# Performance work log

Hardware: AMD Instinct MI355X
Metric: run time of the kernel (lower is better)

Reference implementation:

```python
import jax, jax.numpy as jnp
import numpy as np

NUM_HEADS = 8
EPS = 1e-6


def hamilton(a, b):
    # Quaternion (Hamilton) product on the last axis (size 4), broadcasting leading dims.
    aw, ax, ay, az = a[..., 0], a[..., 1], a[..., 2], a[..., 3]
    bw, bx, by, bz = b[..., 0], b[..., 1], b[..., 2], b[..., 3]
    return jnp.stack([
        aw * bw - ax * bx - ay * by - az * bz,
        aw * bx + ax * bw + ay * bz - az * by,
        aw * by - ax * bz + ay * bw + az * bx,
        aw * bz + ax * by - ay * bx + az * bw,
    ], axis=-1)


def setup_inputs() -> dict:
    key = jax.random.key(0)
    ks = jax.random.split(key, 7)
    B, L, E = 2, 384, 512
    s = 1.0 / np.sqrt(E)
    return {
        'x': jax.random.normal(ks[0], (B, L, E), dtype=jnp.float32),
        'Wq': jax.random.normal(ks[1], (E, E), dtype=jnp.float32) * s,
        'Wk': jax.random.normal(ks[2], (E, E), dtype=jnp.float32) * s,
        'Wv': jax.random.normal(ks[3], (E, E), dtype=jnp.float32) * s,
        'Wo': jax.random.normal(ks[4], (E, E), dtype=jnp.float32) * s,
        'dde_w': jax.random.normal(ks[5], (4, 4), dtype=jnp.float32) * 0.5,
        'dde_b': jnp.zeros((4,), dtype=jnp.float32),
    }


def reference(x, Wq, Wk, Wv, Wo, dde_w, dde_b):
    B, L, E = x.shape
    H = NUM_HEADS
    hd = E // H            # head_dim
    c = hd // 4            # quaternion atoms per head

    def proj_quat(W):
        # x @ W^T  -> split heads -> quaternion atoms: (B*H, L, c, 4)
        y = jnp.einsum('ble,fe->blf', x, W)
        y = y.reshape(B, L, H, hd).transpose(0, 2, 1, 3)  # (B,H,L,hd)
        return y.reshape(B * H, L, c, 4)

    q = proj_quat(Wq)
    k = proj_quat(Wk)
    v = proj_quat(Wv)

    # Broadcasted Hamilton product: (BH, L, L, c, 4)
    interference = hamilton(q[:, :, None, :, :], k[:, None, :, :, :])
    norm = jnp.linalg.norm(interference, axis=-1, keepdims=True) + EPS
    spinor = interference / norm

    # Discrete decision gate: mean over atoms -> (BH, L, L, 4) -> sigmoid(linear)
    gate_in = spinor.mean(axis=-2)
    gate = jax.nn.sigmoid(jnp.einsum('blmq,pq->blmp', gate_in, dde_w) + dde_b)
    spinor = spinor * gate[:, :, :, None, :]

    # Value aggregation: Hamilton product with v, summed over key positions j
    ctx = hamilton(spinor, v[:, None, :, :, :]).sum(axis=2)  # (BH, L, c, 4)

    ctx = ctx.reshape(B, H, L, hd).transpose(0, 2, 1, 3).reshape(B, L, E)
    return jnp.einsum('ble,fe->blf', ctx, Wo)
```

## Files before the change

### kernel.cpp

```cpp
#include <hip/hip_runtime.h>
#include <math.h>

#define L_SEQ 384
#define E_DIM 512
#define NHEAD 8
#define NBH   16
#define HD    64
#define LOG2E 1.44269504f

typedef __attribute__((ext_vector_type(8))) __bf16 bf16x8;
typedef __attribute__((ext_vector_type(8))) _Float16 f16x8;
typedef __attribute__((ext_vector_type(4))) float f32x4;

union u4h8 { uint4 u; f16x8 h; };

__device__ __forceinline__ float uniform_f(float v) {
  return __uint_as_float(__builtin_amdgcn_readfirstlane(__float_as_uint(v)));
}

__device__ __forceinline__ unsigned f2bf(float f) {
  unsigned u = __float_as_uint(f);
  return (u + 0x7FFFu + ((u >> 16) & 1u)) >> 16;
}

__device__ __forceinline__ unsigned ror16(unsigned x) { return (x >> 16) | (x << 16); }

__device__ __forceinline__ float dpp_xor1(float x) {
  return __int_as_float(__builtin_amdgcn_mov_dpp(__float_as_int(x), 0xB1, 0xF, 0xF, 0));
}
__device__ __forceinline__ float dpp_xor2(float x) {
  return __int_as_float(__builtin_amdgcn_mov_dpp(__float_as_int(x), 0x4E, 0xF, 0xF, 0));
}
template <int PAT>
__device__ __forceinline__ float quad_bcast(float x) {
  return __int_as_float(__builtin_amdgcn_mov_dpp(__float_as_int(x), PAT, 0xF, 0xF, 0));
}
template <int IMM>
__device__ __forceinline__ float swz_xor(float x) {
  return __int_as_float(__builtin_amdgcn_ds_swizzle(__float_as_int(x), IMM));
}

__device__ __forceinline__ size_t pidx(int row, int k, int Kd) {
  return ((((size_t)(row >> 4) * (Kd >> 5) + (k >> 5)) * 4 + ((k >> 3) & 3)) * 16
          + (row & 15)) * 8 + (k & 7);
}

__global__ __launch_bounds__(256) void to_bf16_all(
    const float* __restrict__ x, const float* __restrict__ Wq,
    const float* __restrict__ Wk, const float* __restrict__ Wv,
    const float* __restrict__ Wo, unsigned short* __restrict__ dst1,
    unsigned short* __restrict__ dst2, float* __restrict__ outz)
{
  int e0 = (blockIdx.x * 256 + threadIdx.x) * 4;
  if (e0 >= 1835008) return;
  if (e0 >= 1441792) {
    *(float4*)(outz + (e0 - 1441792)) = make_float4(0.f, 0.f, 0.f, 0.f);
    return;
  }
  const float* src; unsigned short* d; int s;
  if (e0 < 393216)       { src = x;  s = e0;           d = dst1; }
  else if (e0 < 655360)  { src = Wq; s = e0 - 393216;  d = dst1 + 393216; }
  else if (e0 < 917504)  { src = Wk; s = e0 - 655360;  d = dst1 + 655360; }
  else if (e0 < 1179648) { src = Wv; s = e0 - 917504;  d = dst1 + 917504; }
  else                   { src = Wo; s = e0 - 1179648; d = dst2; }
  float4 v = *(const float4*)(src + s);
  unsigned lo = f2bf(v.x) | (f2bf(v.y) << 16);
  unsigned hi = f2bf(v.z) | (f2bf(v.w) << 16);
  int row = s >> 9, k = s & 511;
  *(uint2*)(d + pidx(row, k, 512)) = make_uint2(lo, hi);
}

__global__ __launch_bounds__(256) void gemm_qkv(
    const __bf16* __restrict__ A, const __bf16* __restrict__ B0,
    const __bf16* __restrict__ B1, const __bf16* __restrict__ B2,
    _Float16* __restrict__ qhh, _Float16* __restrict__ khh,
    _Float16* __restrict__ Z0)
{
  const int z = blockIdx.z;
  const int tid = threadIdx.x;
  const int wave = tid >> 6, lane = tid & 63;
  const int m0 = blockIdx.y * 64 + wave * 16;
  const int n0 = blockIdx.x * 16;
  const int mr = lane & 15, quad = lane >> 4;
  const int KT = 16;

  const __bf16* ap = A + (size_t)(m0 >> 4) * KT * 512 + lane * 8;
  const int n = n0 + mr;

  if (z == 0) {
    const __bf16* bp = B0 + (size_t)(n0 >> 4) * KT * 512 + lane * 8;
    f32x4 acc = (f32x4){0.f, 0.f, 0.f, 0.f};
    #pragma unroll 4
    for (int ks = 0; ks < KT; ++ks) {
      bf16x8 a = *(const bf16x8*)(ap + (size_t)ks * 512);
      bf16x8 b = *(const bf16x8*)(bp + (size_t)ks * 512);
      acc = __builtin_amdgcn_mfma_f32_16x16x32_bf16(a, b, acc, 0, 0, 0);
    }
    #pragma unroll
    for (int r = 0; r < 4; ++r) {
      float val = acc[r];
      float s = val * val;
      s += dpp_xor1(s);
      s += dpp_xor2(s);
      float sc = __builtin_amdgcn_rsqf(fmaxf(s, 1e-30f));
      int m = m0 + quad * 4 + r;
      int b = m / L_SEQ, l = m - b * L_SEQ;
      int row = (b * NHEAD + (n >> 6)) * L_SEQ + l;
      qhh[pidx(row, n & 63, 64)] = (_Float16)(val * sc);
    }
  } else {
    const __bf16* bpk = B1 + (size_t)(n0 >> 4) * KT * 512 + lane * 8;
    const __bf16* bpv = B2 + (size_t)(n0 >> 4) * KT * 512 + lane * 8;
    f32x4 accK = (f32x4){0.f, 0.f, 0.f, 0.f};
    f32x4 accV = (f32x4){0.f, 0.f, 0.f, 0.f};
    #pragma unroll 4
    for (int ks = 0; ks < KT; ++ks) {
      bf16x8 a = *(const bf16x8*)(ap + (size_t)ks * 512);
      bf16x8 bk = *(const bf16x8*)(bpk + (size_t)ks * 512);
      bf16x8 bv = *(const bf16x8*)(bpv + (size_t)ks * 512);
      accK = __builtin_amdgcn_mfma_f32_16x16x32_bf16(a, bk, accK, 0, 0, 0);
      accV = __builtin_amdgcn_mfma_f32_16x16x32_bf16(a, bv, accV, 0, 0, 0);
    }
    const int a_atom = (n & 63) >> 2, comp = n & 3;
    #pragma unroll
    for (int r = 0; r < 4; ++r) {
      float vk = accK[r], vv = accV[r];
      float s = vk * vk;
      s += dpp_xor1(s);
      s += dpp_xor2(s);
      float kn = vk * __builtin_amdgcn_rsqf(fmaxf(s, 1e-30f));
      int m = m0 + quad * 4 + r;
      int b = m / L_SEQ, l = m - b * L_SEQ;
      int bh = b * NHEAD + (n >> 6);
      int row = bh * L_SEQ + l;
      khh[pidx(row, n & 63, 64)] = (_Float16)kn;
      float v0 = quad_bcast<0x00>(vv), v1 = quad_bcast<0x55>(vv);
      float v2 = quad_bcast<0xAA>(vv), v3 = quad_bcast<0xFF>(vv);
      _Float16* zp = Z0 + (size_t)bh * (256 * 384);
      int colb = a_atom * 16 + comp * 4;
      zp[pidx(colb + 0, l, 384)] = (_Float16)(kn * v0);
      zp[pidx(colb + 1, l, 384)] = (_Float16)(kn * v1);
      zp[pidx(colb + 2, l, 384)] = (_Float16)(kn * v2);
      zp[pidx(colb + 3, l, 384)] = (_Float16)(kn * v3);
    }
  }
}

__global__ __launch_bounds__(256) void gate_pv(
    const _Float16* __restrict__ qhh, const _Float16* __restrict__ khh,
    const _Float16* __restrict__ Z0, const float* __restrict__ dde_w,
    const float* __restrict__ dde_b, const __bf16* __restrict__ Wob,
    float* __restrict__ out)
{
  __shared__ _Float16 gbuf[2][4096];
  __shared__ float qs[16][65];
  __shared__ __bf16 ctx_lds[16][72];

  const int tid = threadIdx.x, w = tid >> 6, lane = tid & 63;
  const int mr = lane & 15, quad = lane >> 4;
  const int bh = blockIdx.y, ib = blockIdx.x;
  const int i0 = ib * 16;

  {
    int il = tid >> 4, k4 = (tid & 15) * 4;
    union { uint2 u; _Float16 h[4]; } cv;
    cv.u = *(const uint2*)(qhh + pidx(bh * L_SEQ + i0 + il, k4, 64));
    qs[il][k4 + 0] = (float)cv.h[0]; qs[il][k4 + 1] = (float)cv.h[1];
    qs[il][k4 + 2] = (float)cv.h[2]; qs[il][k4 + 3] = (float)cv.h[3];
  }

  float wn[16], bn[4];
  #pragma unroll
  for (int t = 0; t < 16; ++t) wn[t] = uniform_f(dde_w[t]) * (-LOG2E * 0.0625f);
  #pragma unroll
  for (int c = 0; c < 4; ++c) bn[c] = uniform_f(dde_b[c]) * (-LOG2E);

  u4h8 fr[4][2];
  {
    const _Float16* ap = qhh + ((size_t)(bh * 24 + ib)) * 2 * 512 + lane * 8;
    #pragma unroll
    for (int ks = 0; ks < 2; ++ks) {
      uint4 qa = *(const uint4*)(ap + ks * 512);
      unsigned s0 = ror16(qa.x), s1 = ror16(qa.y), s2 = ror16(qa.z), s3 = ror16(qa.w);
      fr[0][ks].u = make_uint4(qa.x ^ 0x80000000u, qa.y ^ 0x80008000u,
                               qa.z ^ 0x80000000u, qa.w ^ 0x80008000u);
      fr[1][ks].u = make_uint4(s0, s1 ^ 0x00008000u, s2, s3 ^ 0x00008000u);
      fr[2][ks].u = make_uint4(qa.y, qa.x ^ 0x80000000u, qa.w, qa.z ^ 0x80000000u);
      fr[3][ks].u = make_uint4(s1 ^ 0x80000000u, s0, s3 ^ 0x80000000u, s2);
    }
  }

  const int bq = mr >> 2, e = mr & 3;
  unsigned msk[4];
  #pragma unroll
  for (int c = 0; c < 4; ++c)
    msk[c] = ((((0x284Eu >> (c * 4 + bq)) ^ (0xC6A0u >> (c * 4 + e))) & 1u) << 31);

  f32x4 acc[4][4];
  #pragma unroll
  for (int c = 0; c < 4; ++c)
    #pragma unroll
    for (int nt = 0; nt < 4; ++nt) acc[c][nt] = (f32x4){0.f, 0.f, 0.f, 0.f};

  const int jl = w * 16 + mr;
  const int gw = (jl >> 3) * 128 + (jl & 7) + quad * 32;

  u4h8 kbp[2][2];
  {
    const _Float16* bp = khh + ((size_t)(bh * 24 + w)) * 2 * 512 + lane * 8;
    kbp[0][0].h = *(const f16x8*)(bp);
    kbp[0][1].h = *(const f16x8*)(bp + 512);
  }

  #pragma unroll
  for (int ch = 0; ch < 6; ++ch) {
    const int cur = ch & 1, nxt = cur ^ 1;
    u4h8 zb[2][4];
    #pragma unroll
    for (int ks2 = 0; ks2 < 2; ++ks2)
      #pragma unroll
      for (int nt = 0; nt < 4; ++nt)
        zb[ks2][nt].h = *(const f16x8*)(Z0 + (size_t)bh * (256 * 384)
                         + (((size_t)(w * 4 + nt) * 12 + ch * 2 + ks2) * 512) + lane * 8);

    f32x4 accS[4];
    #pragma unroll
    for (int c = 0; c < 4; ++c) {
      accS[c] = (f32x4){0.f, 0.f, 0.f, 0.f};
      accS[c] = __builtin_amdgcn_mfma_f32_16x16x32_f16(fr[c][0].h, kbp[cur][0].h, accS[c], 0, 0, 0);
      accS[c] = __builtin_amdgcn_mfma_f32_16x16x32_f16(fr[c][1].h, kbp[cur][1].h, accS[c], 0, 0, 0);
    }

    if (ch < 5) {
      const _Float16* bp = khh + ((size_t)(bh * 24 + (ch + 1) * 4 + w)) * 2 * 512 + lane * 8;
      kbp[nxt][0].h = *(const f16x8*)(bp);
      kbp[nxt][1].h = *(const f16x8*)(bp + 512);
    }

    #pragma unroll
    for (int r = 0; r < 4; ++r) {
      float S0 = accS[0][r], S1 = accS[1][r], S2 = accS[2][r], S3 = accS[3][r];
      #pragma unroll
      for (int c = 0; c < 4; ++c) {
        float n = bn[c] + wn[c*4+0]*S0 + wn[c*4+1]*S1 + wn[c*4+2]*S2 + wn[c*4+3]*S3;
        float g = __builtin_amdgcn_rcpf(1.f + __builtin_amdgcn_exp2f(n));
        gbuf[cur][c * 1024 + gw + r * 8] = (_Float16)g;
      }
    }
    __syncthreads();

    #pragma unroll
    for (int ks2 = 0; ks2 < 2; ++ks2) {
      #pragma unroll
      for (int c = 0; c < 4; ++c) {
        f16x8 aa = *(const f16x8*)&gbuf[cur][c * 1024 + ks2 * 512 + lane * 8];
        #pragma unroll
        for (int nt = 0; nt < 4; ++nt)
          acc[c][nt] = __builtin_amdgcn_mfma_f32_16x16x32_f16(aa, zb[ks2][nt].h, acc[c][nt], 0, 0, 0);
      }
    }
  }

  #pragma unroll
  for (int nt = 0; nt < 4; ++nt) {
    #pragma unroll
    for (int r = 0; r < 4; ++r) {
      int il = quad * 4 + r;
      float pb[4];
      #pragma unroll
      for (int c = 0; c < 4; ++c) {
        float sq = __uint_as_float(
            __float_as_uint(qs[il][w * 16 + nt * 4 + (bq ^ c)]) ^ msk[c]);
        float v = sq * acc[c][nt][r];
        v += swz_xor<0x101F>(v);
        v += swz_xor<0x201F>(v);
        pb[c] = v;
      }
      float q0 = pb[0] + dpp_xor1(pb[1]);
      float q1 = pb[1] + dpp_xor1(pb[0]);
      float q2 = pb[2] + dpp_xor1(pb[3]);
      float q3 = pb[3] + dpp_xor1(pb[2]);
      float r0 = q0 + dpp_xor2(q2);
      float r1 = q1 + dpp_xor2(q3);
      float r2 = q2 + dpp_xor2(q0);
      float r3 = q3 + dpp_xor2(q1);
      if (mr == 0) {
        ctx_lds[il][w * 16 + nt * 4 + 0] = (__bf16)r0;
        ctx_lds[il][w * 16 + nt * 4 + 1] = (__bf16)r1;
        ctx_lds[il][w * 16 + nt * 4 + 2] = (__bf16)r2;
        ctx_lds[il][w * 16 + nt * 4 + 3] = (__bf16)r3;
      }
    }
  }
  __syncthreads();

  const int bb_ = bh >> 3, hh = bh & 7;
  const int m_base = bb_ * L_SEQ + i0;
  bf16x8 af[2];
  #pragma unroll
  for (int ks2 = 0; ks2 < 2; ++ks2)
    af[ks2] = *(const bf16x8*)&ctx_lds[mr][ks2 * 32 + quad * 8];
  #pragma unroll
  for (int nt2 = 0; nt2 < 8; ++nt2) {
    const int ntile = w * 8 + nt2;
    f32x4 accO = (f32x4){0.f, 0.f, 0.f, 0.f};
    #pragma unroll
    for (int ks2 = 0; ks2 < 2; ++ks2) {
      bf16x8 b = *(const bf16x8*)(Wob + ((size_t)ntile * 16 + hh * 2 + ks2) * 512 + lane * 8);
      accO = __builtin_amdgcn_mfma_f32_16x16x32_bf16(af[ks2], b, accO, 0, 0, 0);
    }
    const int n = ntile * 16 + mr;
    #pragma unroll
    for (int r = 0; r < 4; ++r) {
      int m = m_base + quad * 4 + r;
      __hip_atomic_fetch_add(&out[(size_t)m * E_DIM + n], accO[r],
                             __ATOMIC_RELAXED, __HIP_MEMORY_SCOPE_AGENT);
    }
  }
}

extern "C" void kernel_launch(void* const* d_in, const int* in_sizes, int n_in,
                              void* d_out, int out_size, void* d_ws, size_t ws_size,
                              hipStream_t stream)
{
  const float* x     = (const float*)d_in[0];
  const float* Wq    = (const float*)d_in[1];
  const float* Wk    = (const float*)d_in[2];
  const float* Wv    = (const float*)d_in[3];
  const float* Wo    = (const float*)d_in[4];
  const float* dde_w = (const float*)d_in[5];
  const float* dde_b = (const float*)d_in[6];
  float* out = (float*)d_out;

  char* ws = (char*)d_ws;
  unsigned short* Wob  = (unsigned short*)(ws + 0);
  _Float16* qhh = (_Float16*)(ws + 524288);
  _Float16* khh = (_Float16*)(ws + 1310720);
  _Float16* Z0h = (_Float16*)(ws + 2097152);
  unsigned short* xb  = (unsigned short*)(ws + 6029312);
  unsigned short* Wqb = (unsigned short*)(ws + 6815744);
  unsigned short* Wkb = (unsigned short*)(ws + 7340032);
  unsigned short* Wvb = (unsigned short*)(ws + 7864320);

  to_bf16_all<<<1792, 256, 0, stream>>>(x, Wq, Wk, Wv, Wo, xb, Wob, out);

  gemm_qkv<<<dim3(32, 12, 2), 256, 0, stream>>>(
      (const __bf16*)xb, (const __bf16*)Wqb, (const __bf16*)Wkb, (const __bf16*)Wvb,
      qhh, khh, Z0h);

  gate_pv<<<dim3(24, 16), 256, 0, stream>>>(
      qhh, khh, Z0h, dde_w, dde_b, (const __bf16*)Wob, out);
}
```

Baseline: 101.3 us.

## Split gate_pv key range across two blocks and rebuild query fragments per chunk

The gate_pv grid gains a z dimension of 2, and each block handles half of the key-position chunks (3 of 6). This doubles the block count to fill the GPU better and shorten each block's serial loop. The permuted query fragments are now rebuilt from the two raw loads right before each MFMA group instead of being kept in 8 registers. The launch bound asks for 3 blocks per CU to raise occupancy. It relies on the epilogue accumulating partial outputs atomically into the zeroed output, so output-projection work and atomic traffic double.

```diff
diff --git a/kernel.cpp b/kernel.cpp
--- a/kernel.cpp
+++ b/kernel.cpp
@@ -43,6 +43,24 @@
 __device__ __forceinline__ size_t pidx(int row, int k, int Kd) {
   return ((((size_t)(row >> 4) * (Kd >> 5) + (k >> 5)) * 4 + ((k >> 3) & 3)) * 16
           + (row & 15)) * 8 + (k & 7);
+}
+
+template <int C>
+__device__ __forceinline__ u4h8 build_fr(uint4 qa) {
+  u4h8 f;
+  if (C == 0) {
+    f.u = make_uint4(qa.x ^ 0x80000000u, qa.y ^ 0x80008000u,
+                     qa.z ^ 0x80000000u, qa.w ^ 0x80008000u);
+  } else if (C == 1) {
+    f.u = make_uint4(ror16(qa.x), ror16(qa.y) ^ 0x00008000u,
+                     ror16(qa.z), ror16(qa.w) ^ 0x00008000u);
+  } else if (C == 2) {
+    f.u = make_uint4(qa.y, qa.x ^ 0x80000000u, qa.w, qa.z ^ 0x80000000u);
+  } else {
+    f.u = make_uint4(ror16(qa.y) ^ 0x80000000u, ror16(qa.x),
+                     ror16(qa.w) ^ 0x80000000u, ror16(qa.z));
+  }
+  return f;
 }
 
 __global__ __launch_bounds__(256) void to_bf16_all(
@@ -146,7 +164,7 @@
   }
 }
 
-__global__ __launch_bounds__(256) void gate_pv(
+__global__ __launch_bounds__(256, 3) void gate_pv(
     const _Float16* __restrict__ qhh, const _Float16* __restrict__ khh,
     const _Float16* __restrict__ Z0, const float* __restrict__ dde_w,
     const float* __restrict__ dde_b, const __bf16* __restrict__ Wob,
@@ -158,7 +176,7 @@
 
   const int tid = threadIdx.x, w = tid >> 6, lane = tid & 63;
   const int mr = lane & 15, quad = lane >> 4;
-  const int bh = blockIdx.y, ib = blockIdx.x;
+  const int bh = blockIdx.y, ib = blockIdx.x, jh = blockIdx.z;
   const int i0 = ib * 16;
 
   {
@@ -175,19 +193,11 @@
   #pragma unroll
   for (int c = 0; c < 4; ++c) bn[c] = uniform_f(dde_b[c]) * (-LOG2E);
 
-  u4h8 fr[4][2];
+  uint4 qa[2];
   {
     const _Float16* ap = qhh + ((size_t)(bh * 24 + ib)) * 2 * 512 + lane * 8;
-    #pragma unroll
-    for (int ks = 0; ks < 2; ++ks) {
-      uint4 qa = *(const uint4*)(ap + ks * 512);
-      unsigned s0 = ror16(qa.x), s1 = ror16(qa.y), s2 = ror16(qa.z), s3 = ror16(qa.w);
-      fr[0][ks].u = make_uint4(qa.x ^ 0x80000000u, qa.y ^ 0x80008000u,
-                               qa.z ^ 0x80000000u, qa.w ^ 0x80008000u);
-      fr[1][ks].u = make_uint4(s0, s1 ^ 0x00008000u, s2, s3 ^ 0x00008000u);
-      fr[2][ks].u = make_uint4(qa.y, qa.x ^ 0x80000000u, qa.w, qa.z ^ 0x80000000u);
-      fr[3][ks].u = make_uint4(s1 ^ 0x80000000u, s0, s3 ^ 0x80000000u, s2);
-    }
+    qa[0] = *(const uint4*)(ap);
+    qa[1] = *(const uint4*)(ap + 512);
   }
 
   const int bq = mr >> 2, e = mr & 3;
@@ -207,14 +217,15 @@
 
   u4h8 kbp[2][2];
   {
-    const _Float16* bp = khh + ((size_t)(bh * 24 + w)) * 2 * 512 + lane * 8;
+    const _Float16* bp = khh + ((size_t)(bh * 24 + jh * 12 + w)) * 2 * 512 + lane * 8;
     kbp[0][0].h = *(const f16x8*)(bp);
     kbp[0][1].h = *(const f16x8*)(bp + 512);
   }
 
   #pragma unroll
-  for (int ch = 0; ch < 6; ++ch) {
-    const int cur = ch & 1, nxt = cur ^ 1;
+  for (int ci = 0; ci < 3; ++ci) {
+    const int ch = jh * 3 + ci;
+    const int cur = ci & 1, nxt = cur ^ 1;
     u4h8 zb[2][4];
     #pragma unroll
     for (int ks2 = 0; ks2 < 2; ++ks2)
@@ -224,15 +235,28 @@
                          + (((size_t)(w * 4 + nt) * 12 + ch * 2 + ks2) * 512) + lane * 8);
 
     f32x4 accS[4];
-    #pragma unroll
-    for (int c = 0; c < 4; ++c) {
-      accS[c] = (f32x4){0.f, 0.f, 0.f, 0.f};
-      accS[c] = __builtin_amdgcn_mfma_f32_16x16x32_f16(fr[c][0].h, kbp[cur][0].h, accS[c], 0, 0, 0);
-      accS[c] = __builtin_amdgcn_mfma_f32_16x16x32_f16(fr[c][1].h, kbp[cur][1].h, accS[c], 0, 0, 0);
-    }
-
-    if (ch < 5) {
-      const _Float16* bp = khh + ((size_t)(bh * 24 + (ch + 1) * 4 + w)) * 2 * 512 + lane * 8;
+    {
+      u4h8 f00 = build_fr<0>(qa[0]), f01 = build_fr<0>(qa[1]);
+      accS[0] = (f32x4){0.f, 0.f, 0.f, 0.f};
+      accS[0] = __builtin_amdgcn_mfma_f32_16x16x32_f16(f00.h, kbp[cur][0].h, accS[0], 0, 0, 0);
+      accS[0] = __builtin_amdgcn_mfma_f32_16x16x32_f16(f01.h, kbp[cur][1].h, accS[0], 0, 0, 0);
+      u4h8 f10 = build_fr<1>(qa[0]), f11 = build_fr<1>(qa[1]);
+      accS[1] = (f32x4){0.f, 0.f, 0.f, 0.f};
+      accS[1] = __builtin_amdgcn_mfma_f32_16x16x32_f16(f10.h, kbp[cur][0].h, accS[1], 0, 0, 0);
+      accS[1] = __builtin_amdgcn_mfma_f32_16x16x32_f16(f11.h, kbp[cur][1].h, accS[1], 0, 0, 0);
+      u4h8 f20 = build_fr<2>(qa[0]), f21 = build_fr<2>(qa[1]);
+      accS[2] = (f32x4){0.f, 0.f, 0.f, 0.f};
+      accS[2] = __builtin_amdgcn_mfma_f32_16x16x32_f16(f20.h, kbp[cur][0].h, accS[2], 0, 0, 0);
+      accS[2] = __builtin_amdgcn_mfma_f32_16x16x32_f16(f21.h, kbp[cur][1].h, accS[2], 0, 0, 0);
+      u4h8 f30 = build_fr<3>(qa[0]), f31 = build_fr<3>(qa[1]);
+      accS[3] = (f32x4){0.f, 0.f, 0.f, 0.f};
+      accS[3] = __builtin_amdgcn_mfma_f32_16x16x32_f16(f30.h, kbp[cur][0].h, accS[3], 0, 0, 0);
+      accS[3] = __builtin_amdgcn_mfma_f32_16x16x32_f16(f31.h, kbp[cur][1].h, accS[3], 0, 0, 0);
+    }
+
+    if (ci < 2) {
+      const _Float16* bp = khh
+          + ((size_t)(bh * 24 + (ch + 1) * 4 + w)) * 2 * 512 + lane * 8;
       kbp[nxt][0].h = *(const f16x8*)(bp);
       kbp[nxt][1].h = *(const f16x8*)(bp + 512);
     }
@@ -348,6 +372,6 @@
       (const __bf16*)xb, (const __bf16*)Wqb, (const __bf16*)Wkb, (const __bf16*)Wvb,
       qhh, khh, Z0h);
 
-  gate_pv<<<dim3(24, 16), 256, 0, stream>>>(
+  gate_pv<<<dim3(24, 16, 2), 256, 0, stream>>>(
       qhh, khh, Z0h, dde_w, dde_b, (const __bf16*)Wob, out);
 }
```

Measured after the change: 112.4 us. +10.9%, slower.
